# Kernel optimization log

Hardware: AMD Instinct MI355X
Metric: run time of the kernel (lower is better)

The kernel has to match this reference:

```python
import jax, jax.numpy as jnp
import numpy as np

N_NODES = 50000
N_RAND_EDGES = 800000
K_HEADS = 4
D = 64
EPS = 1e-8


def setup_inputs() -> dict:
    key = jax.random.key(0)
    k1, k2, k3, k4, k5, k6 = jax.random.split(key, 6)
    x = jax.random.normal(k1, (N_NODES, D), dtype=jnp.float32)
    # edge_index without self loops (module removes then re-adds them), then append self loops
    dst = jax.random.randint(k2, (N_RAND_EDGES,), 0, N_NODES)
    off = jax.random.randint(k3, (N_RAND_EDGES,), 1, N_NODES)
    src = (dst + off) % N_NODES  # guaranteed src != dst
    loops = jnp.arange(N_NODES)
    adj = jnp.stack([jnp.concatenate([dst, loops]), jnp.concatenate([src, loops])]).astype(jnp.int64)
    e = jax.random.uniform(k4, (N_NODES, K_HEADS), dtype=jnp.float32)
    stdv = 1.0 / np.sqrt(D)
    weights = jax.random.uniform(k5, (K_HEADS, D, D), minval=-stdv, maxval=stdv, dtype=jnp.float32)
    # xavier_uniform(gain=1.414) on [K, 2D, 1]
    bound = 1.414 * np.sqrt(6.0 / (2 * D + 1))
    a = jax.random.uniform(k6, (K_HEADS, 2 * D, 1), minval=-bound, maxval=bound, dtype=jnp.float32)
    return {"x": x, "adj": adj, "e": e, "weights": weights, "a": a}


def reference(x, adj, e, weights, a):
    N = x.shape[0]
    O = weights.shape[2]
    dst, src = adj[0], adj[1]  # aggregation destination = adj[0], source = adj[1]
    # per-head projection: h[k] = x @ weights[k]  -> [K, N, O]
    h = jnp.einsum('nd,kdo->kno', x, weights)
    # split attention vector: edge_h @ a == <h[dst], a[:O]> + <h[src], a[O:]>
    a_dst = a[:, :O, 0]   # [K, O]
    a_src = a[:, O:, 0]   # [K, O]
    alpha_dst = jnp.einsum('kno,ko->kn', h, a_dst)  # [K, N]
    alpha_src = jnp.einsum('kno,ko->kn', h, a_src)  # [K, N]
    logits = jax.nn.leaky_relu(alpha_dst[:, dst] + alpha_src[:, src], 0.01)  # [K, E]
    # global (per-head) max subtraction, as in the original
    edge_e = jnp.exp(logits - jnp.max(logits, axis=1, keepdims=True))  # [K, E]
    seg = lambda v: jax.ops.segment_sum(v, dst, num_segments=N)
    denom = jax.vmap(seg)(edge_e) + EPS                                 # [K, N]
    num = jax.vmap(seg)(edge_e[:, :, None] * h[:, src])                 # [K, N, O]
    outputs = num / denom[:, :, None]                                   # [K, N, O]
    out = jnp.einsum('nk,kno->no', e, outputs)                          # mixture over K
    return out + x  # residual
```

## Files before the change

kernel.cpp:

```cpp
#include <hip/hip_runtime.h>
#include <hip/hip_bf16.h>

#define KH 4
#define DIM 64
#define EPSV 1e-8f
#define CSTRIDE 16

typedef __attribute__((ext_vector_type(8))) short bf16x8;
typedef __attribute__((ext_vector_type(4))) float f32x4;
typedef __attribute__((ext_vector_type(2))) float f32x2;

__device__ __forceinline__ float lrelu(float s) { return s > 0.0f ? s : 0.01f * s; }
__device__ __forceinline__ float blo(unsigned u) { return __uint_as_float(u << 16); }
__device__ __forceinline__ float bhi(unsigned u) { return __uint_as_float(u & 0xFFFF0000u); }
__device__ __forceinline__ unsigned short f2b(float f) {
    unsigned u = __float_as_uint(f);
    u += 0x7FFFu + ((u >> 16) & 1u);
    return (unsigned short)(u >> 16);
}

__device__ __forceinline__ unsigned char f2e4m3(float f) {
    unsigned u = __float_as_uint(f);
    unsigned sgn = (u >> 31) << 7;
    float af = fabsf(f);
    if (af >= 0.015625f) {
        unsigned mag = u & 0x7FFFFFFFu;
        unsigned biased = mag - (120u << 23);
        unsigned em = biased >> 20;
        unsigned rem = biased & 0xFFFFFu;
        em += (rem > 0x80000u) ? 1u : ((rem == 0x80000u) ? (em & 1u) : 0u);
        if (em > 126u) em = 126u;
        return (unsigned char)(sgn | em);
    } else {
        int m = (int)rintf(af * 512.0f);
        if (m >= 8) return (unsigned char)(sgn | 8u);
        return (unsigned char)(sgn | (unsigned)m);
    }
}

__device__ __forceinline__ unsigned pk_e4m3(float a, float b) {
#if __has_builtin(__builtin_amdgcn_cvt_pk_fp8_f32)
    return (unsigned)__builtin_amdgcn_cvt_pk_fp8_f32(a, b, 0, false) & 0xFFFFu;
#else
    return (unsigned)f2e4m3(a) | ((unsigned)f2e4m3(b) << 8);
#endif
}

__device__ __forceinline__ void e4m3x4_to_f32(unsigned v, float& h0, float& h1,
                                              float& h2, float& h3) {
#if __has_builtin(__builtin_amdgcn_cvt_pk_f32_fp8)
    f32x2 lo = __builtin_amdgcn_cvt_pk_f32_fp8(v, false);
    f32x2 hi = __builtin_amdgcn_cvt_pk_f32_fp8(v, true);
    h0 = lo.x; h1 = lo.y; h2 = hi.x; h3 = hi.y;
#else
    auto dec = [](unsigned b) -> float {
        unsigned s = b >> 7, em = b & 0x7Fu;
        float r;
        if (em >= 8u) r = __uint_as_float((em << 20) + (120u << 23));
        else r = (float)em * 0.001953125f;
        return s ? -r : r;
    };
    h0 = dec(v & 0xFF); h1 = dec((v >> 8) & 0xFF);
    h2 = dec((v >> 16) & 0xFF); h3 = dec(v >> 24);
#endif
}

__global__ void __launch_bounds__(256, 4)
k_hidden(const float* __restrict__ x,
         const float* __restrict__ W,
         const float* __restrict__ a,
         unsigned* __restrict__ h8,
         float* __restrict__ adst,
         float* __restrict__ asrc,
         int* __restrict__ cnt, int N) {
    int t = threadIdx.x;
    int gid = blockIdx.x * 256 + t;
    if (gid < N * CSTRIDE) cnt[gid] = 0;
    int k = t >> 6;
    int l = t & 63;
    int s = l & 15;
    int q = l >> 4;
    int n0 = blockIdx.x * 16;

    const float* Wk = W + k * DIM * DIM;
    bf16x8 Bf[4][2];
#pragma unroll
    for (int tile = 0; tile < 4; ++tile)
#pragma unroll
        for (int c = 0; c < 2; ++c) {
            const float* wp = Wk + (size_t)(32 * c + 8 * q) * DIM + 16 * tile + s;
#pragma unroll
            for (int j = 0; j < 8; ++j)
                Bf[tile][c][j] = (short)f2b(wp[(size_t)j * DIM]);
        }
    float ad[4], as_[4];
#pragma unroll
    for (int tile = 0; tile < 4; ++tile) {
        ad[tile]  = a[k * 2 * DIM + 16 * tile + s];
        as_[tile] = a[k * 2 * DIM + DIM + 16 * tile + s];
    }

    bf16x8 Af[2];
#pragma unroll
    for (int c = 0; c < 2; ++c) {
        const float* xp = x + (size_t)(n0 + s) * DIM + 32 * c + 8 * q;
#pragma unroll
        for (int j = 0; j < 8; ++j) Af[c][j] = (short)f2b(xp[j]);
    }

    f32x4 acc[4];
#pragma unroll
    for (int tile = 0; tile < 4; ++tile) {
        acc[tile] = (f32x4){0.f, 0.f, 0.f, 0.f};
#pragma unroll
        for (int c = 0; c < 2; ++c)
            acc[tile] = __builtin_amdgcn_mfma_f32_16x16x32_bf16(
                Af[c], Bf[tile][c], acc[tile], 0, 0, 0);
    }

#pragma unroll
    for (int r = 0; r < 4; ++r) {
        float vd = 0.f, vs = 0.f;
#pragma unroll
        for (int tile = 0; tile < 4; ++tile) {
            vd = fmaf(acc[tile][r], ad[tile], vd);
            vs = fmaf(acc[tile][r], as_[tile], vs);
        }
#pragma unroll
        for (int off = 1; off < 16; off <<= 1) {
            vd += __shfl_xor(vd, off);
            vs += __shfl_xor(vs, off);
        }
        if (s == 0) {
            int n = n0 + 4 * q + r;
            adst[n * KH + k] = vd;
            asrc[n * KH + k] = vs;
        }
    }

    __shared__ unsigned char hb[16 * DIM * KH];
#pragma unroll
    for (int tile = 0; tile < 4; ++tile) {
        unsigned p01 = pk_e4m3(acc[tile][0], acc[tile][1]);
        unsigned p23 = pk_e4m3(acc[tile][2], acc[tile][3]);
        int o = 16 * tile + s;
        int col = (o ^ (q << 4));
#pragma unroll
        for (int r = 0; r < 4; ++r) {
            unsigned byte = (r < 2) ? ((p01 >> (8 * r)) & 0xFFu)
                                    : ((p23 >> (8 * (r - 2))) & 0xFFu);
            int n = 4 * q + r;
            hb[(n * DIM + col) * KH + k] = (unsigned char)byte;
        }
    }
    __syncthreads();
    const unsigned* hb4 = (const unsigned*)hb;
#pragma unroll
    for (int it = 0; it < 4; ++it) {
        int w = it * 256 + t;
        int wp = w ^ ((((unsigned)w >> 8) & 3u) << 4);
        h8[(size_t)n0 * DIM + w] = hb4[wp];
    }
}

__global__ void k_bin(const int* __restrict__ dst, const int* __restrict__ src,
                      const float4* __restrict__ adst4, const float4* __restrict__ asrc4,
                      int* __restrict__ cnt, uint4* __restrict__ slots,
                      int cap, int E) {
    int tid = blockIdx.x * blockDim.x + threadIdx.x;
    if (tid * 2 >= E) return;
    int2 d = ((const int2*)dst)[tid];
    int2 s = ((const int2*)src)[tid];
    int sl0 = atomicAdd(&cnt[d.x * CSTRIDE], 1);
    int sl1 = atomicAdd(&cnt[d.y * CSTRIDE], 1);
    float4 ad0 = adst4[d.x], as0 = asrc4[s.x];
    float4 ad1 = adst4[d.y], as1 = asrc4[s.y];
#define EMIT(sl, dn, sn, ad, as)                                              \
    if (sl < cap) {                                                           \
        uint4 sv;                                                             \
        sv.x = (unsigned)sn;                                                  \
        sv.y = (unsigned)f2b(__expf(lrelu(ad.x + as.x))) |                    \
               ((unsigned)f2b(__expf(lrelu(ad.y + as.y))) << 16);             \
        sv.z = (unsigned)f2b(__expf(lrelu(ad.z + as.z))) |                    \
               ((unsigned)f2b(__expf(lrelu(ad.w + as.w))) << 16);             \
        sv.w = 0u;                                                            \
        slots[(size_t)dn * cap + sl] = sv;                                    \
    }
    EMIT(sl0, d.x, s.x, ad0, as0)
    EMIT(sl1, d.y, s.y, ad1, as1)
#undef EMIT
}

__global__ void __launch_bounds__(256, 8)
k_aggr(const int* __restrict__ cnt, const uint4* __restrict__ slots,
       const unsigned* __restrict__ h8,
       const float* __restrict__ efeat, const float* __restrict__ x,
       float* __restrict__ out, int cap, int N) {
    int n = __builtin_amdgcn_readfirstlane(blockIdx.x * 4 + (threadIdx.x >> 6));
    if (n >= N) return;
    int o = threadIdx.x & 63;
    int deg = cnt[n * CSTRIDE]; if (deg > cap) deg = cap;
    const uint4* bs = slots + (size_t)n * cap;
    float v0 = 0.f, v1 = 0.f, v2 = 0.f, v3 = 0.f;
    float d0 = 0.f, d1 = 0.f, d2 = 0.f, d3 = 0.f;
#define ACC(sv, hv)                                                           \
    {                                                                         \
        float h0, h1, h2, h3;                                                 \
        e4m3x4_to_f32(hv, h0, h1, h2, h3);                                    \
        float w;                                                              \
        w = blo(sv.y); v0 = fmaf(w, h0, v0); d0 += w;                         \
        w = bhi(sv.y); v1 = fmaf(w, h1, v1); d1 += w;                         \
        w = blo(sv.z); v2 = fmaf(w, h2, v2); d2 += w;                         \
        w = bhi(sv.z); v3 = fmaf(w, h3, v3); d3 += w;                         \
    }
    int i = 0;
    for (; i + 4 <= deg; i += 4) {
        uint4 s0 = bs[i + 0], s1 = bs[i + 1], s2 = bs[i + 2], s3 = bs[i + 3];
        unsigned a0 = h8[(size_t)s0.x * DIM + o];
        unsigned a1 = h8[(size_t)s1.x * DIM + o];
        unsigned a2 = h8[(size_t)s2.x * DIM + o];
        unsigned a3 = h8[(size_t)s3.x * DIM + o];
        ACC(s0, a0) ACC(s1, a1) ACC(s2, a2) ACC(s3, a3)
    }
    for (; i < deg; ++i) {
        uint4 sv = bs[i];
        unsigned hv = h8[(size_t)sv.x * DIM + o];
        ACC(sv, hv)
    }
#undef ACC
    float4 ef = ((const float4*)efeat)[n];
    float c0 = ef.x / (d0 + EPSV), c1 = ef.y / (d1 + EPSV);
    float c2 = ef.z / (d2 + EPSV), c3 = ef.w / (d3 + EPSV);
    size_t oi = (size_t)n * DIM + o;
    out[oi] = x[oi] + c0 * v0 + c1 * v1 + c2 * v2 + c3 * v3;
}

extern "C" void kernel_launch(void* const* d_in, const int* in_sizes, int n_in,
                              void* d_out, int out_size, void* d_ws, size_t ws_size,
                              hipStream_t stream) {
    const float* x = (const float*)d_in[0];
    const int* adj = (const int*)d_in[1];
    const float* efeat = (const float*)d_in[2];
    const float* W = (const float*)d_in[3];
    const float* a = (const float*)d_in[4];
    float* out = (float*)d_out;

    int N = in_sizes[0] / DIM;
    int E = in_sizes[1] / 2;
    const int* dst = adj;
    const int* src = adj + E;
    int nbhid = (N + 15) / 16;

    unsigned* h8 = (unsigned*)d_ws;
    float* adst = (float*)(h8 + (size_t)N * DIM);
    float* asrc = adst + (size_t)N * KH;
    int* cnt = (int*)(asrc + (size_t)N * KH);
    uint4* slots = (uint4*)(cnt + (size_t)N * CSTRIDE);
    size_t used = (size_t)((char*)slots - (char*)d_ws);
    int cap = (int)((ws_size - used) / ((size_t)N * 16));
    if (cap > 64) cap = 64;

    k_hidden<<<nbhid, 256, 0, stream>>>(x, W, a, h8, adst, asrc, cnt, N);

    int npair = E / 2;
    k_bin<<<(npair + 255) / 256, 256, 0, stream>>>(dst, src, (const float4*)adst,
                                                   (const float4*)asrc, cnt,
                                                   slots, cap, E);

    k_aggr<<<(N + 3) / 4, 256, 0, stream>>>(cnt, slots, h8, efeat, x, out, cap, N);
}
```

Baseline: 169.0 us.

## Partition edge binning by destination range across XCD-mapped block groups

The binning kernel becomes a grid-stride loop over 2048 blocks split into 8 groups, apparently chosen to match the 8 XCDs of the chip. Each group scans every edge but only handles destinations in its own eighth of the node range, so atomics and slot writes for a node come from one group and can stay in that group's L2. Edge indices are read with nontemporal loads. The cost is that each edge-index pair is read eight times instead of once, and the gains depend on blocks actually being assigned to XCDs round-robin.

```diff
diff --git a/kernel.cpp b/kernel.cpp
--- a/kernel.cpp
+++ b/kernel.cpp
@@ -163,31 +163,43 @@
     }
 }
 
-__global__ void k_bin(const int* __restrict__ dst, const int* __restrict__ src,
-                      const float4* __restrict__ adst4, const float4* __restrict__ asrc4,
-                      int* __restrict__ cnt, uint4* __restrict__ slots,
-                      int cap, int E) {
-    int tid = blockIdx.x * blockDim.x + threadIdx.x;
-    if (tid * 2 >= E) return;
-    int2 d = ((const int2*)dst)[tid];
-    int2 s = ((const int2*)src)[tid];
-    int sl0 = atomicAdd(&cnt[d.x * CSTRIDE], 1);
-    int sl1 = atomicAdd(&cnt[d.y * CSTRIDE], 1);
-    float4 ad0 = adst4[d.x], as0 = asrc4[s.x];
-    float4 ad1 = adst4[d.y], as1 = asrc4[s.y];
-#define EMIT(sl, dn, sn, ad, as)                                              \
-    if (sl < cap) {                                                           \
-        uint4 sv;                                                             \
-        sv.x = (unsigned)sn;                                                  \
-        sv.y = (unsigned)f2b(__expf(lrelu(ad.x + as.x))) |                    \
-               ((unsigned)f2b(__expf(lrelu(ad.y + as.y))) << 16);             \
-        sv.z = (unsigned)f2b(__expf(lrelu(ad.z + as.z))) |                    \
-               ((unsigned)f2b(__expf(lrelu(ad.w + as.w))) << 16);             \
-        sv.w = 0u;                                                            \
-        slots[(size_t)dn * cap + sl] = sv;                                    \
-    }
-    EMIT(sl0, d.x, s.x, ad0, as0)
-    EMIT(sl1, d.y, s.y, ad1, as1)
+__global__ void __launch_bounds__(256, 8)
+k_bin(const long long* __restrict__ dstp, const long long* __restrict__ srcp,
+      const float4* __restrict__ adst4, const float4* __restrict__ asrc4,
+      int* __restrict__ cnt, uint4* __restrict__ slots,
+      int cap, int E, int psz) {
+    int p   = blockIdx.x & 7;
+    int bp  = blockIdx.x >> 3;
+    int nbp = (int)(gridDim.x >> 3);
+    int npair = E >> 1;
+    int lo = p * psz;
+    int stride = nbp * 256;
+#define EMIT(dn, sn)                                                          \
+    if ((unsigned)((dn) - lo) < (unsigned)psz) {                              \
+        int sl = atomicAdd(&cnt[(dn) * CSTRIDE], 1);                          \
+        if (sl < cap) {                                                       \
+            float4 ad = adst4[dn];                                            \
+            float4 as = asrc4[sn];                                            \
+            uint4 sv;                                                         \
+            sv.x = (unsigned)(sn);                                            \
+            sv.y = (unsigned)f2b(__expf(lrelu(ad.x + as.x))) |                \
+                   ((unsigned)f2b(__expf(lrelu(ad.y + as.y))) << 16);         \
+            sv.z = (unsigned)f2b(__expf(lrelu(ad.z + as.z))) |                \
+                   ((unsigned)f2b(__expf(lrelu(ad.w + as.w))) << 16);         \
+            sv.w = 0u;                                                        \
+            slots[(size_t)(dn) * cap + sl] = sv;                              \
+        }                                                                     \
+    }
+    for (int i = bp * 256 + (int)threadIdx.x; i < npair; i += stride) {
+        long long dp = __builtin_nontemporal_load(&dstp[i]);
+        long long sp = __builtin_nontemporal_load(&srcp[i]);
+        int d0 = (int)(unsigned)(dp & 0xFFFFFFFFll);
+        int d1 = (int)(unsigned)(((unsigned long long)dp) >> 32);
+        int s0 = (int)(unsigned)(sp & 0xFFFFFFFFll);
+        int s1 = (int)(unsigned)(((unsigned long long)sp) >> 32);
+        EMIT(d0, s0)
+        EMIT(d1, s1)
+    }
 #undef EMIT
 }
 
@@ -262,10 +274,10 @@
 
     k_hidden<<<nbhid, 256, 0, stream>>>(x, W, a, h8, adst, asrc, cnt, N);
 
-    int npair = E / 2;
-    k_bin<<<(npair + 255) / 256, 256, 0, stream>>>(dst, src, (const float4*)adst,
-                                                   (const float4*)asrc, cnt,
-                                                   slots, cap, E);
+    int psz = (N + 7) / 8;
+    k_bin<<<2048, 256, 0, stream>>>((const long long*)dst, (const long long*)src,
+                                    (const float4*)adst, (const float4*)asrc,
+                                    cnt, slots, cap, E, psz);
 
     k_aggr<<<(N + 3) / 4, 256, 0, stream>>>(cnt, slots, h8, efeat, x, out, cap, N);
 }
```

New measurement: 186.0 us. +10.1%, slower.
